# Kernel tuning notes

Hardware: AMD Instinct MI355X
Metric: run time of the kernel (lower is better)

Reference implementation:

```python
import jax, jax.numpy as jnp
import numpy as np

HID, H, D = 128, 4, 32
NB, NP, NC = 60000, 2000, 4000
EM, EP, EI = 150000, 300000, 150000


def segment_softmax(logits, seg, n):
    # logits: [E, H], seg: [E] destination ids
    m = jax.ops.segment_max(logits, seg, num_segments=n)
    m = jnp.where(jnp.isfinite(m), m, 0.0)  # guard empty segments
    e = jnp.exp(logits - m[seg])
    s = jax.ops.segment_sum(e, seg, num_segments=n)
    return e / (s[seg] + 1e-16)


def layer_norm(x, g, b):
    mu = x.mean(-1, keepdims=True)
    v = ((x - mu) ** 2).mean(-1, keepdims=True)
    return (x - mu) / jnp.sqrt(v + 1e-5) * g + b


def setup_inputs():
    key = jax.random.key(0)
    ks = jax.random.split(key, 40)
    i = iter(range(40))
    nrm = lambda shape, s=1.0: jax.random.normal(ks[next(i)], shape, jnp.float32) * s
    w = lambda shape: nrm(shape, 0.05)
    inp = {
        'x_ball': nrm((NB, HID)),
        'x_player': nrm((NP, HID)),
        'x_context': nrm((NC, HID)),
        'em': jnp.stack([jax.random.randint(ks[next(i)], (EM,), 0, NP),
                         jax.random.randint(ks[next(i)], (EM,), 0, NB)]),
        'ep': jnp.stack([jax.random.randint(ks[next(i)], (EP,), 0, NB),
                         jax.random.randint(ks[next(i)], (EP,), 0, NB)]),
        'ei': jnp.stack([jax.random.randint(ks[next(i)], (EI,), 0, NB),
                         jax.random.randint(ks[next(i)], (EI,), 0, NC)]),
        'ea_p': nrm((EP, 1)),
        # GATv2Conv (player -matchup-> ball)
        'g_Wl': w((HID, HID)), 'g_Wr': w((HID, HID)), 'g_att': w((H, D)), 'g_b': jnp.zeros((HID,), jnp.float32),
        # TransformerConv (ball -recent_precedes-> ball), edge_dim=1
        't_Wq': w((HID, HID)), 't_bq': jnp.zeros((HID,), jnp.float32),
        't_Wk': w((HID, HID)), 't_bk': jnp.zeros((HID,), jnp.float32),
        't_Wv': w((HID, HID)), 't_bv': jnp.zeros((HID,), jnp.float32),
        't_We': w((1, HID)),
        't_Wskip': w((HID, HID)), 't_bskip': jnp.zeros((HID,), jnp.float32),
        # SAGEConv mean (ball -informs-> context)
        's_Wl': w((HID, HID)), 's_bl': jnp.zeros((HID,), jnp.float32), 's_Wr': w((HID, HID)),
        # per-type LayerNorms (only applied to types produced by the conv)
        'ln_ball_g': jnp.ones((HID,), jnp.float32), 'ln_ball_b': jnp.zeros((HID,), jnp.float32),
        'ln_ctx_g': jnp.ones((HID,), jnp.float32), 'ln_ctx_b': jnp.zeros((HID,), jnp.float32),
    }
    return inp


def reference(x_ball, x_player, x_context, em, ep, ei, ea_p,
              g_Wl, g_Wr, g_att, g_b,
              t_Wq, t_bq, t_Wk, t_bk, t_Wv, t_bv, t_We, t_Wskip, t_bskip,
              s_Wl, s_bl, s_Wr,
              ln_ball_g, ln_ball_b, ln_ctx_g, ln_ctx_b):
    # ---- GATv2Conv: player -> ball ----
    src, dst = em[0], em[1]
    xl = (x_player @ g_Wl).reshape(NP, H, D)   # src transform
    xr = (x_ball @ g_Wr).reshape(NB, H, D)     # dst transform
    e = xl[src] + xr[dst]                      # [EM, H, D]
    e = jnp.where(e > 0, e, 0.2 * e)           # leaky_relu(0.2)
    logit = jnp.einsum('ehd,hd->eh', e, g_att)
    alpha = segment_softmax(logit, dst, NB)
    gat = jax.ops.segment_sum(xl[src] * alpha[..., None], dst, num_segments=NB)
    gat = gat.reshape(NB, HID) + g_b

    # ---- TransformerConv: ball -> ball, edge_dim=1 ----
    src, dst = ep[0], ep[1]
    q = (x_ball @ t_Wq + t_bq).reshape(NB, H, D)
    k = (x_ball @ t_Wk + t_bk).reshape(NB, H, D)
    v = (x_ball @ t_Wv + t_bv).reshape(NB, H, D)
    ee = (ea_p @ t_We).reshape(EP, H, D)       # lin_edge (no bias)
    kj = k[src] + ee
    logit = jnp.einsum('ehd,ehd->eh', q[dst], kj) / jnp.sqrt(jnp.float32(D))
    alpha = segment_softmax(logit, dst, NB)
    tr = jax.ops.segment_sum((v[src] + ee) * alpha[..., None], dst, num_segments=NB)
    tr = tr.reshape(NB, HID) + x_ball @ t_Wskip + t_bskip  # root/skip connection

    # ---- SAGEConv mean: ball -> context ----
    src, dst = ei[0], ei[1]
    summ = jax.ops.segment_sum(x_ball[src], dst, num_segments=NC)
    cnt = jax.ops.segment_sum(jnp.ones((EI,), jnp.float32), dst, num_segments=NC)
    mean = summ / jnp.maximum(cnt, 1.0)[:, None]
    sage = mean @ s_Wl + s_bl + x_context @ s_Wr

    # ---- HeteroConv aggr='sum' + residual + per-type LayerNorm ----
    ball_out = layer_norm(gat + tr + x_ball, ln_ball_g, ln_ball_b)
    ctx_out = layer_norm(sage + x_context, ln_ctx_g, ln_ctx_b)
    # 'player' receives no messages -> passed through unchanged
    return (ball_out, ctx_out, x_player)
```

## Files before the change

kernel.cpp:

```cpp
#include <hip/hip_runtime.h>
#include <hip/hip_bf16.h>

#define NB 60000
#define NP 2000
#define NC 4000
#define EM_N 150000
#define EP_N 300000
#define EI_N 150000
#define POOL_N (EM_N + EP_N + EI_N)
#define SEG_TOT (NB + NB + NC)
#define SCAN_BLK 1024
#define NPART ((SEG_TOT + SCAN_BLK - 1) / SCAN_BLK)
#define BALL_BLKS ((NB + 63) / 64)
#define PLYR_BLKS ((NP + 63) / 64)
#define CTXG_BLKS ((NC + 63) / 64)
#define GEMM_BLKS (BALL_BLKS + PLYR_BLKS + CTXG_BLKS)
#define FILL_BLKS ((POOL_N + 255) / 256)
#define COPY_BLKS ((NP * 128 + 255) / 256)
#define BBALL ((NB + 3) / 4)

#define QSCALE (0.17677669529663687f * 1.4426950408889634f)
#define LOG2E 1.4426950408889634f

typedef __hip_bfloat16 bf16;
typedef unsigned int u32;
typedef __attribute__((ext_vector_type(8))) short s8v;
typedef __attribute__((ext_vector_type(4))) float f4v;

__device__ __forceinline__ short f2bs(float f) {
    bf16 h = __float2bfloat16(f);
    return __builtin_bit_cast(short, h);
}
__device__ __forceinline__ float bsToF(short s) {
    return __builtin_bit_cast(float, ((unsigned)(unsigned short)s) << 16);
}
__device__ __forceinline__ float loF(u32 v) { return bsToF((short)(v & 0xffff)); }
__device__ __forceinline__ float hiF(u32 v) { return bsToF((short)(v >> 16)); }
__device__ __forceinline__ u32 packbf(float a, float b) {
    return (u32)(unsigned short)f2bs(a) | ((u32)(unsigned short)f2bs(b) << 16);
}
__device__ __forceinline__ void gl_lds16(const void* g, void* l) {
    __builtin_amdgcn_global_load_lds((const __attribute__((address_space(1))) void*)g,
                                     (__attribute__((address_space(3))) void*)l, 16, 0, 0);
}

__global__ void hist_wt_copy_kernel(const int* __restrict__ em, const int* __restrict__ ep,
                                    const int* __restrict__ ei, int* __restrict__ counts,
                                    const float* __restrict__ W0, const float* __restrict__ W1,
                                    const float* __restrict__ W2, const float* __restrict__ W3,
                                    const float* __restrict__ W4, const float* __restrict__ W5,
                                    const float* __restrict__ W6, const float* __restrict__ W7,
                                    ushort* __restrict__ Wt,
                                    const float* __restrict__ x_player, float* __restrict__ out) {
    if (blockIdx.x >= FILL_BLKS) {
        int t = (blockIdx.x - FILL_BLKS) * 256 + threadIdx.x;
        if (t < NP * 128) out[(size_t)(NB + NC) * 128 + t] = x_player[t];
        return;
    }
    int t = blockIdx.x * 256 + threadIdx.x;
    if (t < 8 * 16384) {
        int w = t >> 14, r = t & 16383, k = r >> 7, n = r & 127;
        const float* W = (w == 0) ? W0 : (w == 1) ? W1 : (w == 2) ? W2 : (w == 3) ? W3
                       : (w == 4) ? W4 : (w == 5) ? W5 : (w == 6) ? W6 : W7;
        int sc = (n >> 5) * 32 + ((n & 1) << 4) + ((n & 31) >> 1);
        Wt[w * 16384 + (k >> 3) * 1024 + sc * 8 + (k & 7)] = (unsigned short)f2bs(W[k * 128 + n]);
    }
    if (t < EM_N) atomicAdd(&counts[em[EM_N + t]], 1);
    else if (t < EM_N + EP_N) atomicAdd(&counts[NB + ep[EP_N + (t - EM_N)]], 1);
    else if (t < POOL_N) atomicAdd(&counts[2 * NB + ei[EI_N + (t - EM_N - EP_N)]], 1);
}

__global__ void scan_fused_kernel(const int* __restrict__ counts, int* __restrict__ offsets,
                                  int* __restrict__ cursors, int* __restrict__ gbase) {
    __shared__ int sd[256];
    __shared__ int sbase;
    int b = blockIdx.x, tid = threadIdx.x;
    int base = b * SCAN_BLK + tid * 4;
    int v[4]; int ts = 0;
#pragma unroll
    for (int j = 0; j < 4; j++) { int idx = base + j; v[j] = (idx < SEG_TOT) ? counts[idx] : 0; ts += v[j]; }
    sd[tid] = ts;
    for (int off = 1; off < 256; off <<= 1) {
        __syncthreads(); int t = (tid >= off) ? sd[tid - off] : 0;
        __syncthreads(); sd[tid] += t;
    }
    __syncthreads();
    if (tid == 255) sbase = atomicAdd(gbase, sd[255]);
    __syncthreads();
    int run = sd[tid] - ts + sbase;
#pragma unroll
    for (int j = 0; j < 4; j++) {
        int idx = base + j;
        if (idx < SEG_TOT) { offsets[idx] = run; cursors[idx] = run; }
        run += v[j];
    }
}

__device__ __forceinline__ void pass_compute(const ushort* __restrict__ ldsb, const s8v a[4],
                                             const float* __restrict__ bp,
                                             const float* __restrict__ Ares, float scale,
                                             int mbase, int M, int l16, int quad,
                                             u32* __restrict__ op) {
#pragma unroll
    for (int t = 0; t < 4; t++) {
        f4v alo = {0.f, 0.f, 0.f, 0.f}, ahi = {0.f, 0.f, 0.f, 0.f};
#pragma unroll
        for (int kt = 0; kt < 4; kt++) {
            s8v blo = *(const s8v*)(ldsb + (kt * 4 + quad) * 1024 + (t * 32 + l16) * 8);
            s8v bhi = *(const s8v*)(ldsb + (kt * 4 + quad) * 1024 + (t * 32 + 16 + l16) * 8);
            alo = __builtin_amdgcn_mfma_f32_16x16x32_bf16(a[kt], blo, alo, 0, 0, 0);
            ahi = __builtin_amdgcn_mfma_f32_16x16x32_bf16(a[kt], bhi, ahi, 0, 0, 0);
        }
        float bvlo = 0.f, bvhi = 0.f;
        if (bp) { float2 b2 = ((const float2*)bp)[t * 16 + l16]; bvlo = b2.x; bvhi = b2.y; }
#pragma unroll
        for (int r = 0; r < 4; r++) {
            int row = mbase + quad * 4 + r;
            if (row < M) {
                float vlo = (alo[r] + bvlo) * scale, vhi = (ahi[r] + bvhi) * scale;
                if (Ares) {
                    float2 xr2 = ((const float2*)Ares)[(size_t)row * 64 + t * 16 + l16];
                    vlo += xr2.x; vhi += xr2.y;
                }
                op[(size_t)row * 64 + t * 16 + l16] = packbf(vlo, vhi);
            }
        }
    }
}

__global__ __launch_bounds__(256) void gemm6_fill_kernel(
    const float* __restrict__ Aball, const float* __restrict__ Aplyr, const float* __restrict__ Actx,
    const ushort* __restrict__ Wt,
    const float* __restrict__ bq, const float* __restrict__ bk,
    const float* __restrict__ bv_, const float* __restrict__ bskip,
    const float* __restrict__ g_b, const float* __restrict__ bl,
    u32* __restrict__ xrP, u32* __restrict__ qP, uint2* __restrict__ kvP,
    u32* __restrict__ skipP, u32* __restrict__ xlP, u32* __restrict__ xwP,
    u32* __restrict__ ctxlinP,
    const int* __restrict__ em, const int* __restrict__ ep, const int* __restrict__ ei,
    const float* __restrict__ ea_p, int* __restrict__ cursors, int2* __restrict__ pool) {
    __shared__ ushort lds[2][16384];
    if (blockIdx.x >= GEMM_BLKS) {
        int t = (blockIdx.x - GEMM_BLKS) * 256 + threadIdx.x;
        int seg, s; float ea = 0.f;
        if (t < EM_N) { s = em[t]; seg = em[EM_N + t]; }
        else if (t < EM_N + EP_N) { int e = t - EM_N; s = ep[e]; seg = NB + ep[EP_N + e]; ea = ea_p[e]; }
        else if (t < POOL_N) { int e = t - EM_N - EP_N; s = ei[e]; seg = 2 * NB + ei[EI_N + e]; }
        else return;
        int pos = atomicAdd(&cursors[seg], 1);
        pool[pos] = make_int2(s, __float_as_int(ea));
        return;
    }
    const int tid = threadIdx.x;
    const int lane = tid & 63;
    const int wv = tid >> 6;
    const int quad = lane >> 4, l16 = lane & 15;
    int kind, bidx;
    if (blockIdx.x < BALL_BLKS) { kind = 0; bidx = blockIdx.x; }
    else if (blockIdx.x < BALL_BLKS + PLYR_BLKS) { kind = 1; bidx = blockIdx.x - BALL_BLKS; }
    else { kind = 2; bidx = blockIdx.x - BALL_BLKS - PLYR_BLKS; }
    const int M = (kind == 0) ? NB : (kind == 1) ? NP : NC;
    const float* A = (kind == 0) ? Aball : (kind == 1) ? Aplyr : Actx;
    const int mbase = bidx * 64 + wv * 16;
    const int ldsbase = wv * 512;

#define STAGE(W, BUF) do { \
    const ushort* _src = Wt + (W) * 16384; \
    _Pragma("unroll") \
    for (int p = 0; p < 8; p++) \
        gl_lds16(_src + (size_t)(p * 256 + tid) * 8, (BUF) + p * 2048 + ldsbase); \
} while (0)

    STAGE(kind == 0 ? 0 : (kind == 1 ? 5 : 7), lds[0]);

    s8v a[4];
    {
        int row = mbase + l16;
        if (row >= M) row = M - 1;
        const float* ap = A + (size_t)row * 128 + quad * 8;
#pragma unroll
        for (int kt = 0; kt < 4; kt++) {
            const float4* p = (const float4*)(ap + kt * 32);
            float4 u = p[0], v = p[1];
            s8v f;
            f[0] = f2bs(u.x); f[1] = f2bs(u.y); f[2] = f2bs(u.z); f[3] = f2bs(u.w);
            f[4] = f2bs(v.x); f[5] = f2bs(v.y); f[6] = f2bs(v.z); f[7] = f2bs(v.w);
            a[kt] = f;
        }
    }
    __syncthreads();

    if (kind == 1) {
        pass_compute(lds[0], a, nullptr, nullptr, 1.f, mbase, M, l16, quad, xlP);
        return;
    }
    if (kind == 2) {
        pass_compute(lds[0], a, bl, Actx, 1.f, mbase, M, l16, quad, ctxlinP);
        return;
    }
    STAGE(1, lds[1]);
    pass_compute(lds[0], a, nullptr, nullptr, 1.f, mbase, M, l16, quad, xrP);
    __syncthreads();
    STAGE(2, lds[0]);
    pass_compute(lds[1], a, bq, nullptr, QSCALE, mbase, M, l16, quad, qP);
    __syncthreads();
    STAGE(3, lds[1]);
    u32 kpk[4][4];
#pragma unroll
    for (int t = 0; t < 4; t++) {
        f4v alo = {0.f, 0.f, 0.f, 0.f}, ahi = {0.f, 0.f, 0.f, 0.f};
#pragma unroll
        for (int kt = 0; kt < 4; kt++) {
            s8v blo = *(const s8v*)(lds[0] + (kt * 4 + quad) * 1024 + (t * 32 + l16) * 8);
            s8v bhi = *(const s8v*)(lds[0] + (kt * 4 + quad) * 1024 + (t * 32 + 16 + l16) * 8);
            alo = __builtin_amdgcn_mfma_f32_16x16x32_bf16(a[kt], blo, alo, 0, 0, 0);
            ahi = __builtin_amdgcn_mfma_f32_16x16x32_bf16(a[kt], bhi, ahi, 0, 0, 0);
        }
        float2 bk2 = ((const float2*)bk)[t * 16 + l16];
#pragma unroll
        for (int r = 0; r < 4; r++) kpk[t][r] = packbf(alo[r] + bk2.x, ahi[r] + bk2.y);
    }
    __syncthreads();
    STAGE(4, lds[0]);
#pragma unroll
    for (int t = 0; t < 4; t++) {
        f4v alo = {0.f, 0.f, 0.f, 0.f}, ahi = {0.f, 0.f, 0.f, 0.f};
#pragma unroll
        for (int kt = 0; kt < 4; kt++) {
            s8v blo = *(const s8v*)(lds[1] + (kt * 4 + quad) * 1024 + (t * 32 + l16) * 8);
            s8v bhi = *(const s8v*)(lds[1] + (kt * 4 + quad) * 1024 + (t * 32 + 16 + l16) * 8);
            alo = __builtin_amdgcn_mfma_f32_16x16x32_bf16(a[kt], blo, alo, 0, 0, 0);
            ahi = __builtin_amdgcn_mfma_f32_16x16x32_bf16(a[kt], bhi, ahi, 0, 0, 0);
        }
        float2 bv2 = ((const float2*)bv_)[t * 16 + l16];
#pragma unroll
        for (int r = 0; r < 4; r++) {
            int row = mbase + quad * 4 + r;
            if (row < NB)
                kvP[(size_t)row * 64 + t * 16 + l16] =
                    make_uint2(kpk[t][r], packbf(alo[r] + bv2.x, ahi[r] + bv2.y));
        }
    }
    __syncthreads();
    STAGE(6, lds[1]);
    pass_compute(lds[0], a, bskip, Aball, 1.f, mbase, M, l16, quad, skipP);
    __syncthreads();
    pass_compute(lds[1], a, nullptr, nullptr, 1.f, mbase, M, l16, quad, xwP);
#undef STAGE
}

__device__ __forceinline__ void gat_batch(const u32 xv[4], const bool ok[4],
                                          float xr0, float xr1, float attx, float atty,
                                          float& n0, float& n1, float& deg) {
    float p[4], xa[4], xb[4];
#pragma unroll
    for (int i = 0; i < 4; i++) {
        xa[i] = loF(xv[i]); xb[i] = hiF(xv[i]);
        float u0 = xa[i] + xr0; u0 = u0 > 0.f ? u0 : 0.2f * u0;
        float u1 = xb[i] + xr1; u1 = u1 > 0.f ? u1 : 0.2f * u1;
        p[i] = u0 * attx + u1 * atty;
    }
#pragma unroll
    for (int m = 1; m <= 8; m <<= 1) {
#pragma unroll
        for (int i = 0; i < 4; i++) p[i] += __shfl_xor(p[i], m);
    }
#pragma unroll
    for (int i = 0; i < 4; i++) {
        p[i] = ok[i] ? exp2f(p[i]) : 0.f;
        n0 += p[i] * xa[i]; n1 += p[i] * xb[i]; deg += p[i];
    }
}

__device__ __forceinline__ void tr_batch(const uint2 kv[4], const float ea[4], const bool ok[4],
                                         float q0, float q1, float dw,
                                         float& sv0, float& sv1, float& spe, float& det) {
    float p[4];
#pragma unroll
    for (int i = 0; i < 4; i++) p[i] = q0 * loF(kv[i].x) + q1 * hiF(kv[i].x);
#pragma unroll
    for (int m = 1; m <= 8; m <<= 1) {
#pragma unroll
        for (int i = 0; i < 4; i++) p[i] += __shfl_xor(p[i], m);
    }
#pragma unroll
    for (int i = 0; i < 4; i++) {
        p[i] = ok[i] ? exp2f(p[i] + ea[i] * dw) : 0.f;
        sv0 += p[i] * loF(kv[i].y); sv1 += p[i] * hiF(kv[i].y);
        spe += p[i] * ea[i]; det += p[i];
    }
}

__global__ __launch_bounds__(256) void ball_sage_kernel(
    const u32* __restrict__ xlP, const u32* __restrict__ xrP, const u32* __restrict__ qP,
    const uint2* __restrict__ kvP, const u32* __restrict__ skipP, const u32* __restrict__ xwP,
    const u32* __restrict__ ctxlinP,
    const float* __restrict__ g_att, const float* __restrict__ g_b, const float* __restrict__ We,
    const int* __restrict__ offsets, const int* __restrict__ counts,
    const int2* __restrict__ pool,
    const float* __restrict__ ln_g, const float* __restrict__ ln_b,
    const float* __restrict__ cg, const float* __restrict__ cb,
    float* __restrict__ out) {
    __shared__ float part[4][128];
    const int wv = threadIdx.x >> 6, l = threadIdx.x & 63;

    if (blockIdx.x >= BBALL) {
        int c = blockIdx.x - BBALL;
        int beg = offsets[2 * NB + c], cnt = counts[2 * NB + c];
        float s0 = 0.f, s1 = 0.f;
        int j = wv;
        if (j < cnt) {
            int i0 = pool[beg + j].x;
            int idx1 = (j + 4 < cnt) ? beg + j + 4 : 0;
            int i1 = pool[idx1].x;
            u32 x0 = xwP[(size_t)i0 * 64 + l];
            u32 x1 = xwP[(size_t)i1 * 64 + l];
            for (; j < cnt; j += 4) {
                int idx2 = (j + 8 < cnt) ? beg + j + 8 : 0;
                int i2 = pool[idx2].x;
                s0 += loF(x0); s1 += hiF(x0);
                x0 = x1;
                x1 = xwP[(size_t)i2 * 64 + l];
            }
        }
        part[wv][l * 2] = s0; part[wv][l * 2 + 1] = s1;
        __syncthreads();
        if (wv == 0) {
            float m = fmaxf((float)cnt, 1.f);
            u32 cl = ctxlinP[(size_t)c * 64 + l];
            float v0 = (part[0][l * 2] + part[1][l * 2] + part[2][l * 2] + part[3][l * 2]) / m + loF(cl);
            float v1 = (part[0][l * 2 + 1] + part[1][l * 2 + 1] + part[2][l * 2 + 1] + part[3][l * 2 + 1]) / m + hiF(cl);
            float s = v0 + v1;
#pragma unroll
            for (int m2 = 1; m2 <= 32; m2 <<= 1) s += __shfl_xor(s, m2);
            float mu = s * (1.f / 128.f);
            float d0 = v0 - mu, d1 = v1 - mu;
            float qv = d0 * d0 + d1 * d1;
#pragma unroll
            for (int m2 = 1; m2 <= 32; m2 <<= 1) qv += __shfl_xor(qv, m2);
            float inv = rsqrtf(qv * (1.f / 128.f) + 1e-5f);
            float2 g2 = ((const float2*)cg)[l];
            float2 b2 = ((const float2*)cb)[l];
            ((float2*)out)[(size_t)(NB + c) * 64 + l] =
                make_float2(d0 * inv * g2.x + b2.x, d1 * inv * g2.y + b2.y);
        }
        return;
    }

    const int d = blockIdx.x * 4 + wv;
    const size_t rowD = (size_t)d * 64;
    const int ds = __builtin_amdgcn_readfirstlane(d);

    u32 xr2 = xrP[rowD + l];
    u32 q2 = qP[rowD + l];
    u32 sk = skipP[rowD + l];

    const int begG = offsets[ds], cntG = counts[ds];
    const int begT = offsets[NB + ds], cntT = counts[NB + ds];
    int gS[8];
#pragma unroll
    for (int i = 0; i < 8; i++) { int idx = (i < cntG) ? begG + i : 0; gS[i] = pool[idx].x; }
    int tS[8]; float tE[8];
#pragma unroll
    for (int i = 0; i < 8; i++) {
        int idx = (i < cntT) ? begT + i : 0;
        int2 pr = pool[idx]; tS[i] = pr.x; tE[i] = __int_as_float(pr.y);
    }

    u32 gx[8];
    if (cntG > 0) {
#pragma unroll
        for (int i = 0; i < 4; i++) gx[i] = xlP[(size_t)gS[i] * 64 + l];
        if (cntG > 4) {
#pragma unroll
            for (int i = 4; i < 8; i++) gx[i] = xlP[(size_t)gS[i] * 64 + l];
        }
    }
    uint2 kva[8];
    if (cntT > 0) {
#pragma unroll
        for (int i = 0; i < 4; i++) kva[i] = kvP[(size_t)tS[i] * 64 + l];
        if (cntT > 4) {
#pragma unroll
            for (int i = 4; i < 8; i++) kva[i] = kvP[(size_t)tS[i] * 64 + l];
        }
    }

    float q0 = loF(q2), q1 = hiF(q2);
    float2 we = ((const float2*)We)[l];
    float dw = q0 * we.x + q1 * we.y;
#pragma unroll
    for (int m = 1; m <= 8; m <<= 1) dw += __shfl_xor(dw, m);

    float2 attv = ((const float2*)g_att)[l];
    float attx = attv.x * LOG2E, atty = attv.y * LOG2E;
    float xr0 = loF(xr2), xr1 = hiF(xr2);
    float n0 = 0.f, n1 = 0.f, deg = 0.f;
    if (cntG > 0) {
        bool ok[4];
#pragma unroll
        for (int i = 0; i < 4; i++) ok[i] = (i < cntG);
        gat_batch(&gx[0], ok, xr0, xr1, attx, atty, n0, n1, deg);
        if (cntG > 4) {
            bool ok2[4];
#pragma unroll
            for (int i = 0; i < 4; i++) ok2[i] = (4 + i < cntG);
            gat_batch(&gx[4], ok2, xr0, xr1, attx, atty, n0, n1, deg);
        }
        for (int j = 8; j < cntG; j += 4) {
            bool ok3[4]; u32 xv[4];
#pragma unroll
            for (int i = 0; i < 4; i++) {
                ok3[i] = (j + i < cntG);
                int idx = ok3[i] ? begG + j + i : 0;
                xv[i] = xlP[(size_t)pool[idx].x * 64 + l];
            }
            gat_batch(xv, ok3, xr0, xr1, attx, atty, n0, n1, deg);
        }
    }
    float gat0 = n0 / (deg + 1e-16f), gat1 = n1 / (deg + 1e-16f);

    float sv0 = 0.f, sv1 = 0.f, spe = 0.f, det = 0.f;
    if (cntT > 0) {
        bool ok[4];
#pragma unroll
        for (int i = 0; i < 4; i++) ok[i] = (i < cntT);
        tr_batch(&kva[0], &tE[0], ok, q0, q1, dw, sv0, sv1, spe, det);
        if (cntT > 4) {
            bool ok2[4];
#pragma unroll
            for (int i = 0; i < 4; i++) ok2[i] = (4 + i < cntT);
            tr_batch(&kva[4], &tE[4], ok2, q0, q1, dw, sv0, sv1, spe, det);
        }
        for (int j = 8; j < cntT; j += 4) {
            bool ok3[4]; uint2 kv[4]; float ea[4];
#pragma unroll
            for (int i = 0; i < 4; i++) {
                ok3[i] = (j + i < cntT);
                int idx = ok3[i] ? begT + j + i : 0;
                int2 pr = pool[idx];
                ea[i] = __int_as_float(pr.y);
                kv[i] = kvP[(size_t)pr.x * 64 + l];
            }
            tr_batch(kv, ea, ok3, q0, q1, dw, sv0, sv1, spe, det);
        }
    }
    float tr0 = (sv0 + spe * we.x) / (det + 1e-16f);
    float tr1 = (sv1 + spe * we.y) / (det + 1e-16f);

    float2 gb2 = ((const float2*)g_b)[l];
    float val0 = loF(sk) + gb2.x + gat0 + tr0;
    float val1 = hiF(sk) + gb2.y + gat1 + tr1;
    float s = val0 + val1;
#pragma unroll
    for (int m = 1; m <= 32; m <<= 1) s += __shfl_xor(s, m);
    float mu = s * (1.f / 128.f);
    float d0 = val0 - mu, d1 = val1 - mu;
    float qv = d0 * d0 + d1 * d1;
#pragma unroll
    for (int m = 1; m <= 32; m <<= 1) qv += __shfl_xor(qv, m);
    float inv = rsqrtf(qv * (1.f / 128.f) + 1e-5f);
    float2 g2 = ((const float2*)ln_g)[l];
    float2 b2 = ((const float2*)ln_b)[l];
    ((float2*)out)[rowD + l] = make_float2(d0 * inv * g2.x + b2.x, d1 * inv * g2.y + b2.y);
}

extern "C" void kernel_launch(void* const* d_in, const int* in_sizes, int n_in,
                              void* d_out, int out_size, void* d_ws, size_t ws_size,
                              hipStream_t stream) {
    const float* x_ball = (const float*)d_in[0];
    const float* x_player = (const float*)d_in[1];
    const float* x_context = (const float*)d_in[2];
    const int* em = (const int*)d_in[3];
    const int* ep = (const int*)d_in[4];
    const int* ei = (const int*)d_in[5];
    const float* ea_p = (const float*)d_in[6];
    const float* g_Wl = (const float*)d_in[7];
    const float* g_Wr = (const float*)d_in[8];
    const float* g_att = (const float*)d_in[9];
    const float* g_b = (const float*)d_in[10];
    const float* t_Wq = (const float*)d_in[11];
    const float* t_bq = (const float*)d_in[12];
    const float* t_Wk = (const float*)d_in[13];
    const float* t_bk = (const float*)d_in[14];
    const float* t_Wv = (const float*)d_in[15];
    const float* t_bv = (const float*)d_in[16];
    const float* t_We = (const float*)d_in[17];
    const float* t_Wskip = (const float*)d_in[18];
    const float* t_bskip = (const float*)d_in[19];
    const float* s_Wl = (const float*)d_in[20];
    const float* s_bl = (const float*)d_in[21];
    const float* s_Wr = (const float*)d_in[22];
    const float* ln_ball_g = (const float*)d_in[23];
    const float* ln_ball_b = (const float*)d_in[24];
    const float* ln_ctx_g = (const float*)d_in[25];
    const float* ln_ctx_b = (const float*)d_in[26];
    float* out = (float*)d_out;

    float* ws = (float*)d_ws;
    size_t o = 0;
    int* counts = (int*)(ws + o);   o += SEG_TOT;
    int* gbase = (int*)(ws + o);    o += 1;
    int* offsets = (int*)(ws + o);  o += SEG_TOT;
    int* cursors = (int*)(ws + o);  o += SEG_TOT;
    if (o & 1) o++;
    int2* pool = (int2*)(ws + o);   o += (size_t)POOL_N * 2;
    o = (o + 3) & ~(size_t)3;
    ushort* Wt = (ushort*)(ws + o); o += (8 * 16384) / 2;
    u32* xlP = (u32*)(ws + o);      o += (size_t)NP * 64;
    u32* xrP = (u32*)(ws + o);      o += (size_t)NB * 64;
    u32* qP = (u32*)(ws + o);       o += (size_t)NB * 64;
    u32* skipP = (u32*)(ws + o);    o += (size_t)NB * 64;
    u32* xwP = (u32*)(ws + o);      o += (size_t)NB * 64;
    u32* ctxlinP = (u32*)(ws + o);  o += (size_t)NC * 64;
    if (o & 1) o++;
    uint2* kvP = (uint2*)(ws + o);  o += (size_t)NB * 128;

    dim3 blk(256);
    hipMemsetAsync(counts, 0, (SEG_TOT + 1) * sizeof(int), stream);
    hist_wt_copy_kernel<<<FILL_BLKS + COPY_BLKS, blk, 0, stream>>>(
        em, ep, ei, counts, g_Wr, t_Wq, t_Wk, t_Wv, t_Wskip, g_Wl, s_Wl, s_Wr, Wt, x_player, out);
    scan_fused_kernel<<<NPART, blk, 0, stream>>>(counts, offsets, cursors, gbase);
    gemm6_fill_kernel<<<GEMM_BLKS + FILL_BLKS, blk, 0, stream>>>(
        x_ball, x_player, x_context, Wt, t_bq, t_bk, t_bv, t_bskip, g_b, s_bl,
        xrP, qP, kvP, skipP, xlP, xwP, ctxlinP, em, ep, ei, ea_p, cursors, pool);
    ball_sage_kernel<<<BBALL + NC, blk, 0, stream>>>(
        xlP, xrP, qP, kvP, skipP, xwP, ctxlinP, g_att, g_b, t_We,
        offsets, counts, pool, ln_ball_g, ln_ball_b, ln_ctx_g, ln_ctx_b, out);
}
```

Measured before the change: 301.3 us.

## Split fused six-weight GEMM into per-weight blocks over multiple row tiles

Each GEMM block now handles a single weight matrix across up to four 64-row tiles, instead of one row tile run through all six ball weights with double-buffered staging. This halves LDS per block and prefetches the next tile's activations while the current tile computes, aiming for higher occupancy and more parallel blocks. It also splits the interleaved K/V buffer into separate K and V arrays, so gathers in the ball kernel issue two 4-byte loads instead of one 8-byte load. In exchange, activations are re-read once per weight (six times for ball rows) instead of once.

```diff
diff --git a/kernel.cpp b/kernel.cpp
--- a/kernel.cpp
+++ b/kernel.cpp
@@ -11,10 +11,14 @@
 #define SEG_TOT (NB + NB + NC)
 #define SCAN_BLK 1024
 #define NPART ((SEG_TOT + SCAN_BLK - 1) / SCAN_BLK)
-#define BALL_BLKS ((NB + 63) / 64)
-#define PLYR_BLKS ((NP + 63) / 64)
-#define CTXG_BLKS ((NC + 63) / 64)
-#define GEMM_BLKS (BALL_BLKS + PLYR_BLKS + CTXG_BLKS)
+#define BALL_TILES ((NB + 63) / 64)
+#define PLYR_TILES ((NP + 63) / 64)
+#define CTX_TILES ((NC + 63) / 64)
+#define TPB 4
+#define BW_CH ((BALL_TILES + TPB - 1) / TPB)
+#define PW_CH ((PLYR_TILES + TPB - 1) / TPB)
+#define CW_CH ((CTX_TILES + TPB - 1) / TPB)
+#define GEMM_BLKS (6 * BW_CH + PW_CH + CW_CH)
 #define FILL_BLKS ((POOL_N + 255) / 256)
 #define COPY_BLKS ((NP * 128 + 255) / 256)
 #define BBALL ((NB + 3) / 4)
@@ -96,50 +100,17 @@
     }
 }
 
-__device__ __forceinline__ void pass_compute(const ushort* __restrict__ ldsb, const s8v a[4],
-                                             const float* __restrict__ bp,
-                                             const float* __restrict__ Ares, float scale,
-                                             int mbase, int M, int l16, int quad,
-                                             u32* __restrict__ op) {
-#pragma unroll
-    for (int t = 0; t < 4; t++) {
-        f4v alo = {0.f, 0.f, 0.f, 0.f}, ahi = {0.f, 0.f, 0.f, 0.f};
-#pragma unroll
-        for (int kt = 0; kt < 4; kt++) {
-            s8v blo = *(const s8v*)(ldsb + (kt * 4 + quad) * 1024 + (t * 32 + l16) * 8);
-            s8v bhi = *(const s8v*)(ldsb + (kt * 4 + quad) * 1024 + (t * 32 + 16 + l16) * 8);
-            alo = __builtin_amdgcn_mfma_f32_16x16x32_bf16(a[kt], blo, alo, 0, 0, 0);
-            ahi = __builtin_amdgcn_mfma_f32_16x16x32_bf16(a[kt], bhi, ahi, 0, 0, 0);
-        }
-        float bvlo = 0.f, bvhi = 0.f;
-        if (bp) { float2 b2 = ((const float2*)bp)[t * 16 + l16]; bvlo = b2.x; bvhi = b2.y; }
-#pragma unroll
-        for (int r = 0; r < 4; r++) {
-            int row = mbase + quad * 4 + r;
-            if (row < M) {
-                float vlo = (alo[r] + bvlo) * scale, vhi = (ahi[r] + bvhi) * scale;
-                if (Ares) {
-                    float2 xr2 = ((const float2*)Ares)[(size_t)row * 64 + t * 16 + l16];
-                    vlo += xr2.x; vhi += xr2.y;
-                }
-                op[(size_t)row * 64 + t * 16 + l16] = packbf(vlo, vhi);
-            }
-        }
-    }
-}
-
 __global__ __launch_bounds__(256) void gemm6_fill_kernel(
     const float* __restrict__ Aball, const float* __restrict__ Aplyr, const float* __restrict__ Actx,
     const ushort* __restrict__ Wt,
     const float* __restrict__ bq, const float* __restrict__ bk,
-    const float* __restrict__ bv_, const float* __restrict__ bskip,
-    const float* __restrict__ g_b, const float* __restrict__ bl,
-    u32* __restrict__ xrP, u32* __restrict__ qP, uint2* __restrict__ kvP,
+    const float* __restrict__ bv_, const float* __restrict__ bskip, const float* __restrict__ bl,
+    u32* __restrict__ xrP, u32* __restrict__ qP, u32* __restrict__ kP, u32* __restrict__ vP,
     u32* __restrict__ skipP, u32* __restrict__ xlP, u32* __restrict__ xwP,
     u32* __restrict__ ctxlinP,
     const int* __restrict__ em, const int* __restrict__ ep, const int* __restrict__ ei,
     const float* __restrict__ ea_p, int* __restrict__ cursors, int2* __restrict__ pool) {
-    __shared__ ushort lds[2][16384];
+    __shared__ ushort lds[16384];
     if (blockIdx.x >= GEMM_BLKS) {
         int t = (blockIdx.x - GEMM_BLKS) * 256 + threadIdx.x;
         int seg, s; float ea = 0.f;
@@ -155,98 +126,106 @@
     const int lane = tid & 63;
     const int wv = tid >> 6;
     const int quad = lane >> 4, l16 = lane & 15;
-    int kind, bidx;
-    if (blockIdx.x < BALL_BLKS) { kind = 0; bidx = blockIdx.x; }
-    else if (blockIdx.x < BALL_BLKS + PLYR_BLKS) { kind = 1; bidx = blockIdx.x - BALL_BLKS; }
-    else { kind = 2; bidx = blockIdx.x - BALL_BLKS - PLYR_BLKS; }
-    const int M = (kind == 0) ? NB : (kind == 1) ? NP : NC;
-    const float* A = (kind == 0) ? Aball : (kind == 1) ? Aplyr : Actx;
-    const int mbase = bidx * 64 + wv * 16;
-    const int ldsbase = wv * 512;
-
-#define STAGE(W, BUF) do { \
-    const ushort* _src = Wt + (W) * 16384; \
-    _Pragma("unroll") \
-    for (int p = 0; p < 8; p++) \
-        gl_lds16(_src + (size_t)(p * 256 + tid) * 8, (BUF) + p * 2048 + ldsbase); \
-} while (0)
-
-    STAGE(kind == 0 ? 0 : (kind == 1 ? 5 : 7), lds[0]);
-
-    s8v a[4];
+
+    int bid = blockIdx.x;
+    int w, tile0, ntiles, M;
+    const float* A;
+    if (bid < 6 * BW_CH) {
+        int widx = bid / BW_CH;
+        w = (widx < 5) ? widx : 6;
+        int chunk = bid - widx * BW_CH;
+        tile0 = chunk * TPB; ntiles = min(TPB, BALL_TILES - tile0); M = NB; A = Aball;
+    } else if (bid < 6 * BW_CH + PW_CH) {
+        w = 5; int chunk = bid - 6 * BW_CH;
+        tile0 = chunk * TPB; ntiles = min(TPB, PLYR_TILES - tile0); M = NP; A = Aplyr;
+    } else {
+        w = 7; int chunk = bid - 6 * BW_CH - PW_CH;
+        tile0 = chunk * TPB; ntiles = min(TPB, CTX_TILES - tile0); M = NC; A = Actx;
+    }
+    u32* op; const float* bp = nullptr; const float* resid = nullptr; float scale = 1.f;
+    switch (w) {
+        case 0: op = xrP; break;
+        case 1: op = qP; bp = bq; scale = QSCALE; break;
+        case 2: op = kP; bp = bk; break;
+        case 3: op = vP; bp = bv_; break;
+        case 4: op = skipP; bp = bskip; resid = Aball; break;
+        case 5: op = xlP; break;
+        case 6: op = xwP; break;
+        default: op = ctxlinP; bp = bl; resid = Actx; break;
+    }
+
     {
-        int row = mbase + l16;
-        if (row >= M) row = M - 1;
-        const float* ap = A + (size_t)row * 128 + quad * 8;
+        const ushort* src = Wt + w * 16384;
+#pragma unroll
+        for (int p = 0; p < 8; p++)
+            gl_lds16(src + (size_t)(p * 256 + tid) * 8, lds + p * 2048 + wv * 512);
+    }
+
+    float2 bias2[4];
+#pragma unroll
+    for (int t = 0; t < 4; t++)
+        bias2[t] = bp ? ((const float2*)bp)[t * 16 + l16] : make_float2(0.f, 0.f);
+
+    float4 rawA[8], rawB[8];
+    {
+        int r0 = tile0 * 64 + wv * 16 + l16; if (r0 >= M) r0 = M - 1;
+        const float* ap = A + (size_t)r0 * 128 + quad * 8;
 #pragma unroll
         for (int kt = 0; kt < 4; kt++) {
-            const float4* p = (const float4*)(ap + kt * 32);
-            float4 u = p[0], v = p[1];
+            rawA[kt * 2] = ((const float4*)(ap + kt * 32))[0];
+            rawA[kt * 2 + 1] = ((const float4*)(ap + kt * 32))[1];
+        }
+    }
+    __syncthreads();
+
+    for (int ti = 0; ti < ntiles; ti++) {
+        int tilebase = (tile0 + ti) * 64;
+        if (ti + 1 < ntiles) {
+            int rn = tilebase + 64 + wv * 16 + l16; if (rn >= M) rn = M - 1;
+            const float* ap = A + (size_t)rn * 128 + quad * 8;
+#pragma unroll
+            for (int kt = 0; kt < 4; kt++) {
+                rawB[kt * 2] = ((const float4*)(ap + kt * 32))[0];
+                rawB[kt * 2 + 1] = ((const float4*)(ap + kt * 32))[1];
+            }
+        }
+        s8v a[4];
+#pragma unroll
+        for (int kt = 0; kt < 4; kt++) {
+            float4 u = rawA[kt * 2], v = rawA[kt * 2 + 1];
             s8v f;
             f[0] = f2bs(u.x); f[1] = f2bs(u.y); f[2] = f2bs(u.z); f[3] = f2bs(u.w);
             f[4] = f2bs(v.x); f[5] = f2bs(v.y); f[6] = f2bs(v.z); f[7] = f2bs(v.w);
             a[kt] = f;
         }
-    }
-    __syncthreads();
-
-    if (kind == 1) {
-        pass_compute(lds[0], a, nullptr, nullptr, 1.f, mbase, M, l16, quad, xlP);
-        return;
-    }
-    if (kind == 2) {
-        pass_compute(lds[0], a, bl, Actx, 1.f, mbase, M, l16, quad, ctxlinP);
-        return;
-    }
-    STAGE(1, lds[1]);
-    pass_compute(lds[0], a, nullptr, nullptr, 1.f, mbase, M, l16, quad, xrP);
-    __syncthreads();
-    STAGE(2, lds[0]);
-    pass_compute(lds[1], a, bq, nullptr, QSCALE, mbase, M, l16, quad, qP);
-    __syncthreads();
-    STAGE(3, lds[1]);
-    u32 kpk[4][4];
-#pragma unroll
-    for (int t = 0; t < 4; t++) {
-        f4v alo = {0.f, 0.f, 0.f, 0.f}, ahi = {0.f, 0.f, 0.f, 0.f};
-#pragma unroll
-        for (int kt = 0; kt < 4; kt++) {
-            s8v blo = *(const s8v*)(lds[0] + (kt * 4 + quad) * 1024 + (t * 32 + l16) * 8);
-            s8v bhi = *(const s8v*)(lds[0] + (kt * 4 + quad) * 1024 + (t * 32 + 16 + l16) * 8);
-            alo = __builtin_amdgcn_mfma_f32_16x16x32_bf16(a[kt], blo, alo, 0, 0, 0);
-            ahi = __builtin_amdgcn_mfma_f32_16x16x32_bf16(a[kt], bhi, ahi, 0, 0, 0);
-        }
-        float2 bk2 = ((const float2*)bk)[t * 16 + l16];
-#pragma unroll
-        for (int r = 0; r < 4; r++) kpk[t][r] = packbf(alo[r] + bk2.x, ahi[r] + bk2.y);
-    }
-    __syncthreads();
-    STAGE(4, lds[0]);
-#pragma unroll
-    for (int t = 0; t < 4; t++) {
-        f4v alo = {0.f, 0.f, 0.f, 0.f}, ahi = {0.f, 0.f, 0.f, 0.f};
-#pragma unroll
-        for (int kt = 0; kt < 4; kt++) {
-            s8v blo = *(const s8v*)(lds[1] + (kt * 4 + quad) * 1024 + (t * 32 + l16) * 8);
-            s8v bhi = *(const s8v*)(lds[1] + (kt * 4 + quad) * 1024 + (t * 32 + 16 + l16) * 8);
-            alo = __builtin_amdgcn_mfma_f32_16x16x32_bf16(a[kt], blo, alo, 0, 0, 0);
-            ahi = __builtin_amdgcn_mfma_f32_16x16x32_bf16(a[kt], bhi, ahi, 0, 0, 0);
-        }
-        float2 bv2 = ((const float2*)bv_)[t * 16 + l16];
-#pragma unroll
-        for (int r = 0; r < 4; r++) {
-            int row = mbase + quad * 4 + r;
-            if (row < NB)
-                kvP[(size_t)row * 64 + t * 16 + l16] =
-                    make_uint2(kpk[t][r], packbf(alo[r] + bv2.x, ahi[r] + bv2.y));
-        }
-    }
-    __syncthreads();
-    STAGE(6, lds[1]);
-    pass_compute(lds[0], a, bskip, Aball, 1.f, mbase, M, l16, quad, skipP);
-    __syncthreads();
-    pass_compute(lds[1], a, nullptr, nullptr, 1.f, mbase, M, l16, quad, xwP);
-#undef STAGE
+        const int mbase = tilebase + wv * 16;
+#pragma unroll
+        for (int t = 0; t < 4; t++) {
+            f4v alo = {0.f, 0.f, 0.f, 0.f}, ahi = {0.f, 0.f, 0.f, 0.f};
+#pragma unroll
+            for (int kt = 0; kt < 4; kt++) {
+                s8v blo = *(const s8v*)(lds + (kt * 4 + quad) * 1024 + (t * 32 + l16) * 8);
+                s8v bhi = *(const s8v*)(lds + (kt * 4 + quad) * 1024 + (t * 32 + 16 + l16) * 8);
+                alo = __builtin_amdgcn_mfma_f32_16x16x32_bf16(a[kt], blo, alo, 0, 0, 0);
+                ahi = __builtin_amdgcn_mfma_f32_16x16x32_bf16(a[kt], bhi, ahi, 0, 0, 0);
+            }
+#pragma unroll
+            for (int r = 0; r < 4; r++) {
+                int row = mbase + quad * 4 + r;
+                if (row < M) {
+                    float vlo = (alo[r] + bias2[t].x) * scale;
+                    float vhi = (ahi[r] + bias2[t].y) * scale;
+                    if (resid) {
+                        float2 x2 = ((const float2*)resid)[(size_t)row * 64 + t * 16 + l16];
+                        vlo += x2.x; vhi += x2.y;
+                    }
+                    op[(size_t)row * 64 + t * 16 + l16] = packbf(vlo, vhi);
+                }
+            }
+        }
+#pragma unroll
+        for (int i = 0; i < 8; i++) rawA[i] = rawB[i];
+    }
 }
 
 __device__ __forceinline__ void gat_batch(const u32 xv[4], const bool ok[4],
@@ -272,12 +251,13 @@
     }
 }
 
-__device__ __forceinline__ void tr_batch(const uint2 kv[4], const float ea[4], const bool ok[4],
+__device__ __forceinline__ void tr_batch(const u32 kk[4], const u32 vv[4],
+                                         const float ea[4], const bool ok[4],
                                          float q0, float q1, float dw,
                                          float& sv0, float& sv1, float& spe, float& det) {
     float p[4];
 #pragma unroll
-    for (int i = 0; i < 4; i++) p[i] = q0 * loF(kv[i].x) + q1 * hiF(kv[i].x);
+    for (int i = 0; i < 4; i++) p[i] = q0 * loF(kk[i]) + q1 * hiF(kk[i]);
 #pragma unroll
     for (int m = 1; m <= 8; m <<= 1) {
 #pragma unroll
@@ -286,14 +266,15 @@
 #pragma unroll
     for (int i = 0; i < 4; i++) {
         p[i] = ok[i] ? exp2f(p[i] + ea[i] * dw) : 0.f;
-        sv0 += p[i] * loF(kv[i].y); sv1 += p[i] * hiF(kv[i].y);
+        sv0 += p[i] * loF(vv[i]); sv1 += p[i] * hiF(vv[i]);
         spe += p[i] * ea[i]; det += p[i];
     }
 }
 
 __global__ __launch_bounds__(256) void ball_sage_kernel(
     const u32* __restrict__ xlP, const u32* __restrict__ xrP, const u32* __restrict__ qP,
-    const uint2* __restrict__ kvP, const u32* __restrict__ skipP, const u32* __restrict__ xwP,
+    const u32* __restrict__ kP, const u32* __restrict__ vP,
+    const u32* __restrict__ skipP, const u32* __restrict__ xwP,
     const u32* __restrict__ ctxlinP,
     const float* __restrict__ g_att, const float* __restrict__ g_b, const float* __restrict__ We,
     const int* __restrict__ offsets, const int* __restrict__ counts,
@@ -376,13 +357,13 @@
             for (int i = 4; i < 8; i++) gx[i] = xlP[(size_t)gS[i] * 64 + l];
         }
     }
-    uint2 kva[8];
+    u32 kk[8], vv[8];
     if (cntT > 0) {
 #pragma unroll
-        for (int i = 0; i < 4; i++) kva[i] = kvP[(size_t)tS[i] * 64 + l];
+        for (int i = 0; i < 4; i++) { kk[i] = kP[(size_t)tS[i] * 64 + l]; vv[i] = vP[(size_t)tS[i] * 64 + l]; }
         if (cntT > 4) {
 #pragma unroll
-            for (int i = 4; i < 8; i++) kva[i] = kvP[(size_t)tS[i] * 64 + l];
+            for (int i = 4; i < 8; i++) { kk[i] = kP[(size_t)tS[i] * 64 + l]; vv[i] = vP[(size_t)tS[i] * 64 + l]; }
         }
     }
 
@@ -425,24 +406,25 @@
         bool ok[4];
 #pragma unroll
         for (int i = 0; i < 4; i++) ok[i] = (i < cntT);
-        tr_batch(&kva[0], &tE[0], ok, q0, q1, dw, sv0, sv1, spe, det);
+        tr_batch(&kk[0], &vv[0], &tE[0], ok, q0, q1, dw, sv0, sv1, spe, det);
         if (cntT > 4) {
             bool ok2[4];
 #pragma unroll
             for (int i = 0; i < 4; i++) ok2[i] = (4 + i < cntT);
-            tr_batch(&kva[4], &tE[4], ok2, q0, q1, dw, sv0, sv1, spe, det);
+            tr_batch(&kk[4], &vv[4], &tE[4], ok2, q0, q1, dw, sv0, sv1, spe, det);
         }
         for (int j = 8; j < cntT; j += 4) {
-            bool ok3[4]; uint2 kv[4]; float ea[4];
+            bool ok3[4]; u32 kt2[4], vt2[4]; float ea[4];
 #pragma unroll
             for (int i = 0; i < 4; i++) {
                 ok3[i] = (j + i < cntT);
                 int idx = ok3[i] ? begT + j + i : 0;
                 int2 pr = pool[idx];
                 ea[i] = __int_as_float(pr.y);
-                kv[i] = kvP[(size_t)pr.x * 64 + l];
+                kt2[i] = kP[(size_t)pr.x * 64 + l];
+                vt2[i] = vP[(size_t)pr.x * 64 + l];
             }
-            tr_batch(kv, ea, ok3, q0, q1, dw, sv0, sv1, spe, det);
+            tr_batch(kt2, vt2, ea, ok3, q0, q1, dw, sv0, sv1, spe, det);
         }
     }
     float tr0 = (sv0 + spe * we.x) / (det + 1e-16f);
@@ -513,8 +495,8 @@
     u32* skipP = (u32*)(ws + o);    o += (size_t)NB * 64;
     u32* xwP = (u32*)(ws + o);      o += (size_t)NB * 64;
     u32* ctxlinP = (u32*)(ws + o);  o += (size_t)NC * 64;
-    if (o & 1) o++;
-    uint2* kvP = (uint2*)(ws + o);  o += (size_t)NB * 128;
+    u32* kP = (u32*)(ws + o);       o += (size_t)NB * 64;
+    u32* vP = (u32*)(ws + o);       o += (size_t)NB * 64;
 
     dim3 blk(256);
     hipMemsetAsync(counts, 0, (SEG_TOT + 1) * sizeof(int), stream);
@@ -522,9 +504,9 @@
         em, ep, ei, counts, g_Wr, t_Wq, t_Wk, t_Wv, t_Wskip, g_Wl, s_Wl, s_Wr, Wt, x_player, out);
     scan_fused_kernel<<<NPART, blk, 0, stream>>>(counts, offsets, cursors, gbase);
     gemm6_fill_kernel<<<GEMM_BLKS + FILL_BLKS, blk, 0, stream>>>(
-        x_ball, x_player, x_context, Wt, t_bq, t_bk, t_bv, t_bskip, g_b, s_bl,
-        xrP, qP, kvP, skipP, xlP, xwP, ctxlinP, em, ep, ei, ea_p, cursors, pool);
+        x_ball, x_player, x_context, Wt, t_bq, t_bk, t_bv, t_bskip, s_bl,
+        xrP, qP, kP, vP, skipP, xlP, xwP, ctxlinP, em, ep, ei, ea_p, cursors, pool);
     ball_sage_kernel<<<BBALL + NC, blk, 0, stream>>>(
-        xlP, xrP, qP, kvP, skipP, xwP, ctxlinP, g_att, g_b, t_We,
+        xlP, xrP, qP, kP, vP, skipP, xwP, ctxlinP, g_att, g_b, t_We,
         offsets, counts, pool, ln_ball_g, ln_ball_b, ln_ctx_g, ln_ctx_b, out);
 }
```

Result: slower. 310.1 us (+2.9%).
